# Kernel optimization log

Measured on AMD Instinct MI355X. Metric: run time of the kernel, lower is better.

## Reference

```python
import jax, jax.numpy as jnp
import numpy as np

B, N, D = 2, 8192, 1024
H, DH = 16, 64
SEG = 512          # total_segment_len (num_longterm_mem_tokens = 0)
P = 16             # num_persist_mem_tokens
EPS = 1.1920929e-07  # torch RMSNorm eps=None -> finfo(float32).eps


def _rope(x, pos, theta=10000.0):
    # rotary-embedding-torch style: interleaved pairs, freqs repeated (n r), r=2
    d = x.shape[-1]
    inv_freq = 1.0 / (theta ** (jnp.arange(0, d, 2, dtype=jnp.float32) / d))  # [d/2]
    ang = pos[:, None] * inv_freq                                             # [n, d/2]
    cos = jnp.repeat(jnp.cos(ang), 2, axis=-1)                                # [n, d]
    sin = jnp.repeat(jnp.sin(ang), 2, axis=-1)
    x1, x2 = x[..., 0::2], x[..., 1::2]
    rot = jnp.stack((-x2, x1), axis=-1).reshape(x.shape)
    return x * cos + rot * sin


def setup_inputs() -> dict:
    key = jax.random.key(0)
    ks = jax.random.split(key, 5)
    return {
        "seq": jax.random.normal(ks[0], (B, N, D), dtype=jnp.float32),
        "w_norm": 1.0 + 0.02 * jax.random.normal(ks[1], (D,), dtype=jnp.float32),
        "Wqkv": jax.random.normal(ks[2], (D, 3 * H * DH), dtype=jnp.float32) * (D ** -0.5),
        "Wout": jax.random.normal(ks[3], (H * DH, D), dtype=jnp.float32) * ((H * DH) ** -0.5),
        "pm": 0.02 * jax.random.normal(ks[4], (2, H, P, DH), dtype=jnp.float32),
    }


def reference(seq, w_norm, Wqkv, Wout, pm):
    b, n, d = seq.shape
    w = n // SEG  # n is a multiple of SEG by construction

    # RMSNorm
    x = seq * jax.lax.rsqrt(jnp.mean(seq * seq, axis=-1, keepdims=True) + EPS) * w_norm

    # QKV projection, split heads -> [b, h, n, dh]
    qkv = x @ Wqkv
    q, k, v = jnp.split(qkv, 3, axis=-1)
    split = lambda t: t.reshape(b, n, H, DH).transpose(0, 2, 1, 3)
    q, k, v = split(q), split(k), split(v)

    # RoPE on full (global) positions before segmenting
    pos = jnp.arange(n, dtype=jnp.float32)
    q = _rope(q, pos)
    k = _rope(k, pos)

    # Segment: [b, h, n, dh] -> [b*w, h, SEG, dh]
    seg = lambda t: t.reshape(b, H, w, SEG, DH).transpose(0, 2, 1, 3, 4).reshape(b * w, H, SEG, DH)
    q, k, v = seg(q), seg(k), seg(v)

    # Prepend persistent memory KVs
    pmk = jnp.broadcast_to(pm[0], (b * w, H, P, DH))
    pmv = jnp.broadcast_to(pm[1], (b * w, H, P, DH))
    k = jnp.concatenate((pmk, k), axis=-2)  # [b*w, h, P+SEG, dh]
    v = jnp.concatenate((pmv, v), axis=-2)

    # Causal attention with kv offset P (persistent tokens always visible)
    scale = DH ** -0.5
    scores = jnp.einsum('bhid,bhjd->bhij', q, k) * scale  # [b*w, h, SEG, P+SEG]
    mask = (jnp.arange(P + SEG) - P)[None, :] <= jnp.arange(SEG)[:, None]
    scores = jnp.where(mask, scores, jnp.finfo(scores.dtype).min)
    attn = jax.nn.softmax(scores, axis=-1)
    out = jnp.einsum('bhij,bhjd->bhid', attn, v)  # [b*w, h, SEG, dh]

    # Merge heads, un-segment, output projection
    out = out.transpose(0, 2, 1, 3).reshape(b * w, SEG, H * DH)
    out = out @ Wout
    out = out.reshape(b, n, -1)
    return out
```

## Files before the change

kernel.cpp:

```cpp
#include <hip/hip_runtime.h>
#include <hip/hip_bf16.h>
#include <stdint.h>
#include <stddef.h>

typedef _Float16 f16;
typedef __attribute__((ext_vector_type(8))) _Float16 f16x8;
typedef __attribute__((ext_vector_type(4))) _Float16 f16x4;
typedef __attribute__((ext_vector_type(4))) float f32x4;
typedef __attribute__((ext_vector_type(16))) float f32x16;

#define MFMA_F16(a, b, c) __builtin_amdgcn_mfma_f32_16x16x32_f16(a, b, c, 0, 0, 0)
#define MFMA32_F16(a, b, c) __builtin_amdgcn_mfma_f32_32x32x16_f16(a, b, c, 0, 0, 0)

#define LOG2_10K_32 0.41524101186092025f

__device__ __forceinline__ uint32_t swz(uint32_t ci) {
    return (ci & ~7u) | ((ci ^ (ci >> 3)) & 7u);
}

__device__ __forceinline__ void async_ld16(void* lds, const void* g) {
    __builtin_amdgcn_global_load_lds(
        (const __attribute__((address_space(1))) void*)g,
        (__attribute__((address_space(3))) void*)lds, 16, 0, 0);
}

__global__ __launch_bounds__(256) void k_transpose_cast(
        const float* __restrict__ S, f16* __restrict__ D, int rows, int cols) {
    __shared__ float tile[32][33];
    int x = threadIdx.x & 31, y = threadIdx.x >> 5;
    int c0 = blockIdx.x * 32, r0 = blockIdx.y * 32;
#pragma unroll
    for (int i = 0; i < 32; i += 8)
        tile[y + i][x] = S[(size_t)(r0 + y + i) * cols + c0 + x];
    __syncthreads();
#pragma unroll
    for (int i = 0; i < 32; i += 8)
        D[(size_t)(c0 + y + i) * rows + r0 + x] = (f16)tile[x][y + i];
}

__global__ __launch_bounds__(256) void k_rmsnorm(
        const float* __restrict__ seq, const float* __restrict__ w, f16* __restrict__ X) {
    int row = blockIdx.x, t = threadIdx.x;
    const float4* sp = (const float4*)(seq + (size_t)row * 1024);
    float4 v = sp[t];
    float ss = v.x * v.x + v.y * v.y + v.z * v.z + v.w * v.w;
#pragma unroll
    for (int off = 32; off >= 1; off >>= 1) ss += __shfl_xor(ss, off, 64);
    __shared__ float red[4];
    if ((t & 63) == 0) red[t >> 6] = ss;
    __syncthreads();
    float tot = red[0] + red[1] + red[2] + red[3];
    float rs = rsqrtf(tot * (1.0f / 1024.0f) + 1.1920929e-07f);
    const float4* wp = (const float4*)w;
    float4 wv = wp[t];
    f16x4 o;
    o[0] = (f16)(v.x * rs * wv.x);
    o[1] = (f16)(v.y * rs * wv.y);
    o[2] = (f16)(v.z * rs * wv.z);
    o[3] = (f16)(v.w * rs * wv.w);
    *(f16x4*)(X + (size_t)row * 1024 + t * 4) = o;
}

__global__ __launch_bounds__(256) void k_gemm_qkv(
        const f16* __restrict__ A, const f16* __restrict__ BT,
        f16* __restrict__ Qb, f16* __restrict__ Kb, f16* __restrict__ Vt) {
    const int K = 1024;
    __shared__ f16 As[128 * 32];
    __shared__ f16 Bs[128 * 32];
    const int t = threadIdx.x;
    const int lane = t & 63, wave = t >> 6, l32 = lane & 31, half = lane >> 5;
    const int m0 = blockIdx.y * 128, n0 = blockIdx.x * 128;
    const int wm = (wave & 1) * 64, wn = (wave >> 1) * 64;
    f32x16 acc[2][2];
#pragma unroll
    for (int i = 0; i < 2; i++)
#pragma unroll
        for (int j = 0; j < 2; j++)
#pragma unroll
            for (int r = 0; r < 16; r++) acc[i][j][r] = 0.f;

    uint32_t aoff[2][2], boff[2][2];
#pragma unroll
    for (int bk = 0; bk < 2; bk++)
#pragma unroll
        for (int ks = 0; ks < 2; ks++) {
            aoff[bk][ks] = swz((uint32_t)(wm + bk * 32 + l32) * 4 + ks * 2 + half) * 16;
            boff[bk][ks] = swz((uint32_t)(wn + bk * 32 + l32) * 4 + ks * 2 + half) * 16;
        }
    uint32_t c0 = swz(t), c1 = swz(t + 256);
    const f16* Ag0 = A + (size_t)(m0 + (c0 >> 2)) * K + (c0 & 3) * 8;
    const f16* Ag1 = A + (size_t)(m0 + (c1 >> 2)) * K + (c1 & 3) * 8;
    const f16* Bg0 = BT + (size_t)(n0 + (c0 >> 2)) * K + (c0 & 3) * 8;
    const f16* Bg1 = BT + (size_t)(n0 + (c1 >> 2)) * K + (c1 & 3) * 8;
    char* AsB = (char*)As;
    char* BsB = (char*)Bs;

    for (int k0 = 0; k0 < K; k0 += 32) {
        __syncthreads();
        async_ld16(AsB + t * 16, Ag0 + k0);
        async_ld16(AsB + (t + 256) * 16, Ag1 + k0);
        async_ld16(BsB + t * 16, Bg0 + k0);
        async_ld16(BsB + (t + 256) * 16, Bg1 + k0);
        __builtin_amdgcn_s_waitcnt(0x0f70);
        __syncthreads();
        f16x8 a[2][2], b[2][2];
#pragma unroll
        for (int bk = 0; bk < 2; bk++)
#pragma unroll
            for (int ks = 0; ks < 2; ks++) {
                a[bk][ks] = *(const f16x8*)(AsB + aoff[bk][ks]);
                b[bk][ks] = *(const f16x8*)(BsB + boff[bk][ks]);
            }
#pragma unroll
        for (int mb = 0; mb < 2; mb++)
#pragma unroll
            for (int nb = 0; nb < 2; nb++) {
                acc[mb][nb] = MFMA32_F16(b[nb][0], a[mb][0], acc[mb][nb]);
                acc[mb][nb] = MFMA32_F16(b[nb][1], a[mb][1], acc[mb][nb]);
            }
    }

    const int region = n0 >> 10;
#pragma unroll
    for (int mb = 0; mb < 2; mb++) {
        int row = m0 + wm + mb * 32 + l32;
        int b_ = row >> 13, n_ = row & 8191;
        int win = n_ >> 9, i_ = n_ & 511;
        float fn = (float)n_;
#pragma unroll
        for (int nb = 0; nb < 2; nb++) {
            int colb = n0 + wn + nb * 32 + half * 4;
            int cr = colb & 1023;
            int h = cr >> 6;
            int d0 = cr & 63;
            int wh = ((b_ * 16 + win) << 4) + h;
            if (region < 2) {
                f16* base = (region == 0)
                    ? (Qb + ((size_t)wh * 512 + i_) * 64)
                    : (Kb + ((size_t)wh * 576 + 16 + i_) * 64);
#pragma unroll
                for (int q = 0; q < 4; q++) {
                    int d = d0 + q * 8;
                    float j0f = (float)(d >> 1);
                    float ang0 = fn * exp2f(-LOG2_10K_32 * j0f);
                    float ang1 = fn * exp2f(-LOG2_10K_32 * (j0f + 1.0f));
                    float s0, c0f, s1, c1f;
                    sincosf(ang0, &s0, &c0f);
                    sincosf(ang1, &s1, &c1f);
                    float x0 = (float)(f16)acc[mb][nb][q * 4 + 0];
                    float x1 = (float)(f16)acc[mb][nb][q * 4 + 1];
                    float x2 = (float)(f16)acc[mb][nb][q * 4 + 2];
                    float x3 = (float)(f16)acc[mb][nb][q * 4 + 3];
                    f16x4 ov;
                    ov[0] = (f16)(x0 * c0f - x1 * s0);
                    ov[1] = (f16)(x1 * c0f + x0 * s0);
                    ov[2] = (f16)(x2 * c1f - x3 * s1);
                    ov[3] = (f16)(x3 * c1f + x2 * s1);
                    *(f16x4*)(base + d) = ov;
                }
            } else {
                f16* vbase = Vt + (size_t)wh * 36864 + 16 + i_;
#pragma unroll
                for (int q = 0; q < 4; q++)
#pragma unroll
                    for (int r = 0; r < 4; r++)
                        vbase[(size_t)(d0 + q * 8 + r) * 576] = (f16)acc[mb][nb][q * 4 + r];
            }
        }
    }
}

__global__ __launch_bounds__(256) void k_gemm_out(
        const f16* __restrict__ A, const f16* __restrict__ BT,
        float* __restrict__ C, int M, int N, int K) {
    __shared__ f16 As[128 * 32];
    __shared__ f16 Bs[128 * 32];
    const int t = threadIdx.x;
    const int lane = t & 63, wave = t >> 6, l32 = lane & 31, half = lane >> 5;
    const int m0 = blockIdx.y * 128, n0 = blockIdx.x * 128;
    const int wm = (wave & 1) * 64, wn = (wave >> 1) * 64;
    f32x16 acc[2][2];
#pragma unroll
    for (int i = 0; i < 2; i++)
#pragma unroll
        for (int j = 0; j < 2; j++)
#pragma unroll
            for (int r = 0; r < 16; r++) acc[i][j][r] = 0.f;

    uint32_t aoff[2][2], boff[2][2];
#pragma unroll
    for (int bk = 0; bk < 2; bk++)
#pragma unroll
        for (int ks = 0; ks < 2; ks++) {
            aoff[bk][ks] = swz((uint32_t)(wm + bk * 32 + l32) * 4 + ks * 2 + half) * 16;
            boff[bk][ks] = swz((uint32_t)(wn + bk * 32 + l32) * 4 + ks * 2 + half) * 16;
        }
    uint32_t c0 = swz(t), c1 = swz(t + 256);
    const f16* Ag0 = A + (size_t)(m0 + (c0 >> 2)) * K + (c0 & 3) * 8;
    const f16* Ag1 = A + (size_t)(m0 + (c1 >> 2)) * K + (c1 & 3) * 8;
    const f16* Bg0 = BT + (size_t)(n0 + (c0 >> 2)) * K + (c0 & 3) * 8;
    const f16* Bg1 = BT + (size_t)(n0 + (c1 >> 2)) * K + (c1 & 3) * 8;
    char* AsB = (char*)As;
    char* BsB = (char*)Bs;

    for (int k0 = 0; k0 < K; k0 += 32) {
        __syncthreads();
        async_ld16(AsB + t * 16, Ag0 + k0);
        async_ld16(AsB + (t + 256) * 16, Ag1 + k0);
        async_ld16(BsB + t * 16, Bg0 + k0);
        async_ld16(BsB + (t + 256) * 16, Bg1 + k0);
        __builtin_amdgcn_s_waitcnt(0x0f70);
        __syncthreads();
        f16x8 a[2][2], b[2][2];
#pragma unroll
        for (int bk = 0; bk < 2; bk++)
#pragma unroll
            for (int ks = 0; ks < 2; ks++) {
                a[bk][ks] = *(const f16x8*)(AsB + aoff[bk][ks]);
                b[bk][ks] = *(const f16x8*)(BsB + boff[bk][ks]);
            }
#pragma unroll
        for (int mb = 0; mb < 2; mb++)
#pragma unroll
            for (int nb = 0; nb < 2; nb++) {
                acc[mb][nb] = MFMA32_F16(b[nb][0], a[mb][0], acc[mb][nb]);
                acc[mb][nb] = MFMA32_F16(b[nb][1], a[mb][1], acc[mb][nb]);
            }
    }
#pragma unroll
    for (int mb = 0; mb < 2; mb++) {
        int row = m0 + wm + mb * 32 + l32;
#pragma unroll
        for (int nb = 0; nb < 2; nb++) {
            int colb = n0 + wn + nb * 32 + half * 4;
#pragma unroll
            for (int q = 0; q < 4; q++) {
                f32x4 ov;
#pragma unroll
                for (int r = 0; r < 4; r++) ov[r] = acc[mb][nb][q * 4 + r];
                *(f32x4*)(C + (size_t)row * N + colb + q * 8) = ov;
            }
        }
    }
}

__global__ __launch_bounds__(256) void k_pmpad(
        const float* __restrict__ pm, f16* __restrict__ Kb, f16* __restrict__ Vt) {
    int wh = blockIdx.x, h = wh & 15, t = threadIdx.x;
    const float* pk = pm + (size_t)h * 1024;
    f16* kb = Kb + (size_t)wh * 36864;
    int e0 = t * 4;
#pragma unroll
    for (int k = 0; k < 4; k++) kb[e0 + k] = (f16)pk[e0 + k];
#pragma unroll
    for (int k = 0; k < 12; k++) kb[33792 + t + k * 256] = (f16)0.f;
    const float* pv = pm + 16384 + (size_t)h * 1024;
    f16* vb = Vt + (size_t)wh * 36864;
    {
        int d = t & 63, s4 = (t >> 6) * 4;
#pragma unroll
        for (int k = 0; k < 4; k++)
            vb[(size_t)d * 576 + s4 + k] = (f16)pv[(s4 + k) * 64 + d];
    }
    {
        int d = t >> 2, rep = t & 3;
#pragma unroll
        for (int m = 0; m < 12; m++)
            vb[(size_t)d * 576 + 528 + rep * 12 + m] = (f16)0.f;
    }
}

__global__ __launch_bounds__(512) void k_attn(
        const f16* __restrict__ Q, const f16* __restrict__ Kb,
        const f16* __restrict__ Vt, f16* __restrict__ AO) {
    const int bid = blockIdx.x;
    const int wh = ((bid >> 5) << 3) | (bid & 7);
    const int pair = (bid >> 3) & 3;
    const int i0 = pair * 128;
    const int t = threadIdx.x, lane = t & 63, wave = t >> 6, quad = lane >> 4, l16 = lane & 15;
    __shared__ f16 Ks[64 * 64];
    __shared__ f16 Vs[64 * 64];
    __shared__ f16 Ps[8][16][80];

    const int ig = i0 + wave * 16 + l16;
    const f16* qptr = Q + ((size_t)wh * 512 + ig) * 64 + quad * 8;
    f16x8 qf0 = *(const f16x8*)(qptr);
    f16x8 qf1 = *(const f16x8*)(qptr + 32);

    const f32x4 zero = {0.f, 0.f, 0.f, 0.f};
    f32x4 o[4];
#pragma unroll
    for (int i = 0; i < 4; i++) o[i] = zero;
    float m_l = -1e30f, l_l = 0.f;

    uint32_t g = swz((uint32_t)t);
    const f16* kg0 = Kb + ((size_t)wh * 576 + (g >> 3)) * 64 + (g & 7) * 8;
    const f16* vg0 = Vt + ((size_t)wh * 64 + (g >> 3)) * 576 + (g & 7) * 8;
    char* KsB = (char*)Ks;
    char* VsB = (char*)Vs;

    uint32_t boff[4][2];
#pragma unroll
    for (int i = 0; i < 4; i++)
#pragma unroll
        for (int f = 0; f < 2; f++)
            boff[i][f] = swz((uint32_t)(i * 16 + l16) * 8 + f * 4 + quad) * 16;

    f16* psrow = &Ps[wave][l16][0];
    int njt = 2 * pair + 3;
    if (njt > 9) njt = 9;

    const int jcap = (ig + 16 < 527) ? (ig + 16) : 527;

    f16x8 kreg = *(const f16x8*)(kg0);
    f16x8 vreg = *(const f16x8*)(vg0);

    for (int jt = 0; jt < njt; jt++) {
        const int j0 = jt * 64;
        __builtin_amdgcn_sched_barrier(0);
        __builtin_amdgcn_s_barrier();
        __builtin_amdgcn_sched_barrier(0);
        *(f16x8*)(KsB + t * 16) = kreg;
        *(f16x8*)(VsB + t * 16) = vreg;
        if (jt + 1 < njt) {
            kreg = *(const f16x8*)(kg0 + (size_t)(j0 + 64) * 64);
            vreg = *(const f16x8*)(vg0 + (j0 + 64));
        }
        __builtin_amdgcn_s_waitcnt(0xc07f);
        __builtin_amdgcn_sched_barrier(0);
        __builtin_amdgcn_s_barrier();
        __builtin_amdgcn_sched_barrier(0);

        f32x4 s[4];
#pragma unroll
        for (int jb = 0; jb < 4; jb++) {
            f16x8 kv0 = *(const f16x8*)(KsB + boff[jb][0]);
            f16x8 kv1 = *(const f16x8*)(KsB + boff[jb][1]);
            f32x4 z = zero;
            z = MFMA_F16(kv0, qf0, z);
            z = MFMA_F16(kv1, qf1, z);
            s[jb] = z;
        }

        const bool fullt = (j0 + 63 <= i0 + wave * 16 + 16) && (j0 + 64 <= 528);
        float mx = -1e30f;
        if (fullt) {
#pragma unroll
            for (int jb = 0; jb < 4; jb++)
#pragma unroll
                for (int r = 0; r < 4; r++) {
                    float val = s[jb][r] * 0.125f;
                    s[jb][r] = val;
                    mx = fmaxf(mx, val);
                }
        } else {
#pragma unroll
            for (int jb = 0; jb < 4; jb++)
#pragma unroll
                for (int r = 0; r < 4; r++) {
                    int jg = j0 + jb * 16 + quad * 4 + r;
                    float val = (jg <= jcap) ? s[jb][r] * 0.125f : -1e30f;
                    s[jb][r] = val;
                    mx = fmaxf(mx, val);
                }
        }
        mx = fmaxf(mx, __shfl_xor(mx, 16, 64));
        mx = fmaxf(mx, __shfl_xor(mx, 32, 64));
        const bool skipresc = __all(mx <= m_l);
        float mnew = fmaxf(m_l, mx);
        float alpha = 1.0f;
        if (!skipresc) alpha = __expf(m_l - mnew);
        m_l = mnew;
        float rsum = 0.f;
#pragma unroll
        for (int jb = 0; jb < 4; jb++) {
            f16x4 pw;
#pragma unroll
            for (int r = 0; r < 4; r++) {
                float p = __expf(s[jb][r] - mnew);
                rsum += p;
                pw[r] = (f16)p;
            }
            *(f16x4*)(psrow + jb * 16 + quad * 4) = pw;
        }
        rsum += __shfl_xor(rsum, 16, 64);
        rsum += __shfl_xor(rsum, 32, 64);
        if (skipresc) {
            l_l = l_l + rsum;
        } else {
            l_l = l_l * alpha + rsum;
#pragma unroll
            for (int nd = 0; nd < 4; nd++) o[nd] *= alpha;
        }

        __builtin_amdgcn_s_waitcnt(0xc07f);
        __builtin_amdgcn_sched_barrier(0);

        f16x8 pb0 = *(const f16x8*)(psrow + quad * 8);
        f16x8 pb1 = *(const f16x8*)(psrow + 32 + quad * 8);
#pragma unroll
        for (int nd = 0; nd < 4; nd++) {
            f16x8 v0 = *(const f16x8*)(VsB + boff[nd][0]);
            f16x8 v1 = *(const f16x8*)(VsB + boff[nd][1]);
            o[nd] = MFMA_F16(v0, pb0, o[nd]);
            o[nd] = MFMA_F16(v1, pb1, o[nd]);
        }
    }

    const int bw = wh >> 4, h = wh & 15;
    float inv = 1.f / l_l;
    f16* dst = AO + ((size_t)bw * 512 + ig) * 1024 + h * 64 + quad * 4;
#pragma unroll
    for (int nd = 0; nd < 4; nd++) {
        f16x4 ov;
#pragma unroll
        for (int r = 0; r < 4; r++) ov[r] = (f16)(o[nd][r] * inv);
        *(f16x4*)(dst + nd * 16) = ov;
    }
}

extern "C" void kernel_launch(void* const* d_in, const int* in_sizes, int n_in,
                              void* d_out, int out_size, void* d_ws, size_t ws_size,
                              hipStream_t stream) {
    const float* seq   = (const float*)d_in[0];
    const float* wnorm = (const float*)d_in[1];
    const float* Wqkv  = (const float*)d_in[2];
    const float* Wout  = (const float*)d_in[3];
    const float* pm    = (const float*)d_in[4];
    float* out = (float*)d_out;
    char* ws = (char*)d_ws;

    f16* WqkvT = (f16*)(ws + 0);
    f16* WoutT = (f16*)(ws + 6291456);
    f16* X     = (f16*)(ws + 8388608);
    f16* Qb    = (f16*)(ws + 41943040);
    f16* AO    = (f16*)(ws + 75497472);
    f16* Kb    = (f16*)(ws + 109051904);
    f16* Vt    = (f16*)(ws + 146800640);

    k_transpose_cast<<<dim3(96, 32), 256, 0, stream>>>(Wqkv, WqkvT, 1024, 3072);
    k_transpose_cast<<<dim3(32, 32), 256, 0, stream>>>(Wout, WoutT, 1024, 1024);
    k_rmsnorm<<<16384, 256, 0, stream>>>(seq, wnorm, X);
    k_pmpad<<<512, 256, 0, stream>>>(pm, Kb, Vt);
    k_gemm_qkv<<<dim3(24, 128), 256, 0, stream>>>(X, WqkvT, Qb, Kb, Vt);
    k_attn<<<2048, 512, 0, stream>>>(Qb, Kb, Vt, AO);
    k_gemm_out<<<dim3(8, 128), 256, 0, stream>>>(AO, WoutT, out, 16384, 1024, 1024);
}
```

Before: 407.4 us.

## Merge prep kernels and rewrite output GEMM with 256x256 tiles and 4-stage pipeline

Fuses the two weight transpose-casts into one launch and folds the persistent-memory padding into the RMSNorm launch, which cuts launch count. The output projection GEMM moves from 128x128 tiles with a single LDS buffer to 256x256 tiles on 512 threads. It adds a 4-stage async global-to-LDS ring with prefetch distance 3, split barriers that overlap loads with MFMA, and setprio around the MFMA groups. The larger tile gives only 256 blocks and needs 128KB of LDS per block, so occupancy and the tail effect become risks.

```diff
diff --git a/kernel.cpp b/kernel.cpp
--- a/kernel.cpp
+++ b/kernel.cpp
@@ -24,11 +24,18 @@
         (__attribute__((address_space(3))) void*)lds, 16, 0, 0);
 }
 
-__global__ __launch_bounds__(256) void k_transpose_cast(
-        const float* __restrict__ S, f16* __restrict__ D, int rows, int cols) {
+__global__ __launch_bounds__(256) void k_prep_w(
+        const float* __restrict__ Wqkv, const float* __restrict__ Wout,
+        f16* __restrict__ WqkvT, f16* __restrict__ WoutT) {
     __shared__ float tile[32][33];
     int x = threadIdx.x & 31, y = threadIdx.x >> 5;
-    int c0 = blockIdx.x * 32, r0 = blockIdx.y * 32;
+    int bx = blockIdx.x;
+    const float* S;
+    f16* D;
+    int rows, cols, bxe;
+    if (bx < 96) { S = Wqkv; D = WqkvT; rows = 1024; cols = 3072; bxe = bx; }
+    else         { S = Wout; D = WoutT; rows = 1024; cols = 1024; bxe = bx - 96; }
+    int c0 = bxe * 32, r0 = blockIdx.y * 32;
 #pragma unroll
     for (int i = 0; i < 32; i += 8)
         tile[y + i][x] = S[(size_t)(r0 + y + i) * cols + c0 + x];
@@ -38,27 +45,53 @@
         D[(size_t)(c0 + y + i) * rows + r0 + x] = (f16)tile[x][y + i];
 }
 
-__global__ __launch_bounds__(256) void k_rmsnorm(
-        const float* __restrict__ seq, const float* __restrict__ w, f16* __restrict__ X) {
-    int row = blockIdx.x, t = threadIdx.x;
-    const float4* sp = (const float4*)(seq + (size_t)row * 1024);
-    float4 v = sp[t];
-    float ss = v.x * v.x + v.y * v.y + v.z * v.z + v.w * v.w;
-#pragma unroll
-    for (int off = 32; off >= 1; off >>= 1) ss += __shfl_xor(ss, off, 64);
+__global__ __launch_bounds__(256) void k_prep_x(
+        const float* __restrict__ seq, const float* __restrict__ w, f16* __restrict__ X,
+        const float* __restrict__ pm, f16* __restrict__ Kb, f16* __restrict__ Vt) {
     __shared__ float red[4];
-    if ((t & 63) == 0) red[t >> 6] = ss;
-    __syncthreads();
-    float tot = red[0] + red[1] + red[2] + red[3];
-    float rs = rsqrtf(tot * (1.0f / 1024.0f) + 1.1920929e-07f);
-    const float4* wp = (const float4*)w;
-    float4 wv = wp[t];
-    f16x4 o;
-    o[0] = (f16)(v.x * rs * wv.x);
-    o[1] = (f16)(v.y * rs * wv.y);
-    o[2] = (f16)(v.z * rs * wv.z);
-    o[3] = (f16)(v.w * rs * wv.w);
-    *(f16x4*)(X + (size_t)row * 1024 + t * 4) = o;
+    const int b = blockIdx.x, t = threadIdx.x;
+    if (b < 16384) {
+        const float4* sp = (const float4*)(seq + (size_t)b * 1024);
+        float4 v = sp[t];
+        float ss = v.x * v.x + v.y * v.y + v.z * v.z + v.w * v.w;
+#pragma unroll
+        for (int off = 32; off >= 1; off >>= 1) ss += __shfl_xor(ss, off, 64);
+        if ((t & 63) == 0) red[t >> 6] = ss;
+        __syncthreads();
+        float tot = red[0] + red[1] + red[2] + red[3];
+        float rs = rsqrtf(tot * (1.0f / 1024.0f) + 1.1920929e-07f);
+        const float4* wp = (const float4*)w;
+        float4 wv = wp[t];
+        f16x4 o;
+        o[0] = (f16)(v.x * rs * wv.x);
+        o[1] = (f16)(v.y * rs * wv.y);
+        o[2] = (f16)(v.z * rs * wv.z);
+        o[3] = (f16)(v.w * rs * wv.w);
+        *(f16x4*)(X + (size_t)b * 1024 + t * 4) = o;
+    } else {
+        int wh = b - 16384, h = wh & 15;
+        const float* pk = pm + (size_t)h * 1024;
+        f16* kb = Kb + (size_t)wh * 36864;
+        int e0 = t * 4;
+#pragma unroll
+        for (int k = 0; k < 4; k++) kb[e0 + k] = (f16)pk[e0 + k];
+#pragma unroll
+        for (int k = 0; k < 12; k++) kb[33792 + t + k * 256] = (f16)0.f;
+        const float* pv = pm + 16384 + (size_t)h * 1024;
+        f16* vb = Vt + (size_t)wh * 36864;
+        {
+            int d = t & 63, s4 = (t >> 6) * 4;
+#pragma unroll
+            for (int k = 0; k < 4; k++)
+                vb[(size_t)d * 576 + s4 + k] = (f16)pv[(s4 + k) * 64 + d];
+        }
+        {
+            int d = t >> 2, rep = t & 3;
+#pragma unroll
+            for (int m = 0; m < 12; m++)
+                vb[(size_t)d * 576 + 528 + rep * 12 + m] = (f16)0.f;
+        }
+    }
 }
 
 __global__ __launch_bounds__(256) void k_gemm_qkv(
@@ -170,65 +203,115 @@
     }
 }
 
-__global__ __launch_bounds__(256) void k_gemm_out(
+__global__ __launch_bounds__(512, 2) void k_gemm_out(
         const f16* __restrict__ A, const f16* __restrict__ BT,
-        float* __restrict__ C, int M, int N, int K) {
-    __shared__ f16 As[128 * 32];
-    __shared__ f16 Bs[128 * 32];
+        float* __restrict__ C, int M, int N, int Kp) {
+    const int K = 1024;
+    const int NT = 32;
+    __shared__ __align__(16) char ldsA[65536];
+    __shared__ __align__(16) char ldsB[65536];
     const int t = threadIdx.x;
     const int lane = t & 63, wave = t >> 6, l32 = lane & 31, half = lane >> 5;
-    const int m0 = blockIdx.y * 128, n0 = blockIdx.x * 128;
-    const int wm = (wave & 1) * 64, wn = (wave >> 1) * 64;
-    f32x16 acc[2][2];
-#pragma unroll
-    for (int i = 0; i < 2; i++)
+    const int m0 = blockIdx.y * 256, n0 = blockIdx.x * 256;
+    const int wm = (wave >> 2) * 128, wn = (wave & 3) * 64;
+
+    f32x16 acc[4][2];
+#pragma unroll
+    for (int i = 0; i < 4; i++)
 #pragma unroll
         for (int j = 0; j < 2; j++)
 #pragma unroll
             for (int r = 0; r < 16; r++) acc[i][j][r] = 0.f;
 
-    uint32_t aoff[2][2], boff[2][2];
-#pragma unroll
-    for (int bk = 0; bk < 2; bk++)
-#pragma unroll
-        for (int ks = 0; ks < 2; ks++) {
-            aoff[bk][ks] = swz((uint32_t)(wm + bk * 32 + l32) * 4 + ks * 2 + half) * 16;
-            boff[bk][ks] = swz((uint32_t)(wn + bk * 32 + l32) * 4 + ks * 2 + half) * 16;
-        }
-    uint32_t c0 = swz(t), c1 = swz(t + 256);
-    const f16* Ag0 = A + (size_t)(m0 + (c0 >> 2)) * K + (c0 & 3) * 8;
-    const f16* Ag1 = A + (size_t)(m0 + (c1 >> 2)) * K + (c1 & 3) * 8;
-    const f16* Bg0 = BT + (size_t)(n0 + (c0 >> 2)) * K + (c0 & 3) * 8;
-    const f16* Bg1 = BT + (size_t)(n0 + (c1 >> 2)) * K + (c1 & 3) * 8;
-    char* AsB = (char*)As;
-    char* BsB = (char*)Bs;
-
-    for (int k0 = 0; k0 < K; k0 += 32) {
-        __syncthreads();
-        async_ld16(AsB + t * 16, Ag0 + k0);
-        async_ld16(AsB + (t + 256) * 16, Ag1 + k0);
-        async_ld16(BsB + t * 16, Bg0 + k0);
-        async_ld16(BsB + (t + 256) * 16, Bg1 + k0);
-        __builtin_amdgcn_s_waitcnt(0x0f70);
-        __syncthreads();
-        f16x8 a[2][2], b[2][2];
-#pragma unroll
-        for (int bk = 0; bk < 2; bk++)
-#pragma unroll
-            for (int ks = 0; ks < 2; ks++) {
-                a[bk][ks] = *(const f16x8*)(AsB + aoff[bk][ks]);
-                b[bk][ks] = *(const f16x8*)(BsB + boff[bk][ks]);
-            }
-#pragma unroll
-        for (int mb = 0; mb < 2; mb++)
-#pragma unroll
-            for (int nb = 0; nb < 2; nb++) {
-                acc[mb][nb] = MFMA32_F16(b[nb][0], a[mb][0], acc[mb][nb]);
-                acc[mb][nb] = MFMA32_F16(b[nb][1], a[mb][1], acc[mb][nb]);
-            }
-    }
-#pragma unroll
-    for (int mb = 0; mb < 2; mb++) {
+    uint32_t aoff[4][2], boff[2][2];
+#pragma unroll
+    for (int mb = 0; mb < 4; mb++)
+#pragma unroll
+        for (int ks = 0; ks < 2; ks++)
+            aoff[mb][ks] = swz((uint32_t)(wm + mb * 32 + l32) * 4 + ks * 2 + half) * 16;
+#pragma unroll
+    for (int nb = 0; nb < 2; nb++)
+#pragma unroll
+        for (int ks = 0; ks < 2; ks++)
+            boff[nb][ks] = swz((uint32_t)(wn + nb * 32 + l32) * 4 + ks * 2 + half) * 16;
+
+    uint32_t g0 = swz((uint32_t)t), g1 = swz((uint32_t)t + 512);
+    const f16* Ag0 = A + (size_t)(m0 + (g0 >> 2)) * K + (g0 & 3) * 8;
+    const f16* Ag1 = A + (size_t)(m0 + (g1 >> 2)) * K + (g1 & 3) * 8;
+    const f16* Bg0 = BT + (size_t)(n0 + (g0 >> 2)) * K + (g0 & 3) * 8;
+    const f16* Bg1 = BT + (size_t)(n0 + (g1 >> 2)) * K + (g1 & 3) * 8;
+
+#pragma unroll
+    for (int p = 0; p < 3; ++p) {
+        char* dA = ldsA + p * 16384;
+        async_ld16(dA + t * 16, Ag0 + p * 32);
+        async_ld16(dA + (t + 512) * 16, Ag1 + p * 32);
+        char* dB = ldsB + p * 16384;
+        async_ld16(dB + t * 16, Bg0 + p * 32);
+        async_ld16(dB + (t + 512) * 16, Bg1 + p * 32);
+    }
+    __builtin_amdgcn_s_waitcnt(0x0f78);
+    __builtin_amdgcn_s_barrier();
+    __builtin_amdgcn_sched_barrier(0);
+
+#pragma unroll 4
+    for (int kt = 0; kt < NT; ++kt) {
+        char* As_s = ldsA + (kt & 3) * 16384;
+        char* Bs_s = ldsB + (kt & 3) * 16384;
+        f16x8 a00 = *(const f16x8*)(As_s + aoff[0][0]);
+        f16x8 a01 = *(const f16x8*)(As_s + aoff[0][1]);
+        f16x8 a10 = *(const f16x8*)(As_s + aoff[1][0]);
+        f16x8 a11 = *(const f16x8*)(As_s + aoff[1][1]);
+        f16x8 b00 = *(const f16x8*)(Bs_s + boff[0][0]);
+        f16x8 b01 = *(const f16x8*)(Bs_s + boff[0][1]);
+        f16x8 b10 = *(const f16x8*)(Bs_s + boff[1][0]);
+        f16x8 b11 = *(const f16x8*)(Bs_s + boff[1][1]);
+        if (kt < NT - 3) {
+            char* dA = ldsA + ((kt + 3) & 3) * 16384;
+            async_ld16(dA + t * 16, Ag0 + (kt + 3) * 32);
+            async_ld16(dA + (t + 512) * 16, Ag1 + (kt + 3) * 32);
+        }
+        __builtin_amdgcn_s_barrier();
+        __builtin_amdgcn_s_setprio(1);
+        acc[0][0] = MFMA32_F16(b00, a00, acc[0][0]);
+        acc[0][0] = MFMA32_F16(b01, a01, acc[0][0]);
+        acc[0][1] = MFMA32_F16(b10, a00, acc[0][1]);
+        acc[0][1] = MFMA32_F16(b11, a01, acc[0][1]);
+        acc[1][0] = MFMA32_F16(b00, a10, acc[1][0]);
+        acc[1][0] = MFMA32_F16(b01, a11, acc[1][0]);
+        acc[1][1] = MFMA32_F16(b10, a10, acc[1][1]);
+        acc[1][1] = MFMA32_F16(b11, a11, acc[1][1]);
+        __builtin_amdgcn_s_setprio(0);
+        __builtin_amdgcn_s_barrier();
+        f16x8 a20 = *(const f16x8*)(As_s + aoff[2][0]);
+        f16x8 a21 = *(const f16x8*)(As_s + aoff[2][1]);
+        f16x8 a30 = *(const f16x8*)(As_s + aoff[3][0]);
+        f16x8 a31 = *(const f16x8*)(As_s + aoff[3][1]);
+        if (kt < NT - 3) {
+            char* dB = ldsB + ((kt + 3) & 3) * 16384;
+            async_ld16(dB + t * 16, Bg0 + (kt + 3) * 32);
+            async_ld16(dB + (t + 512) * 16, Bg1 + (kt + 3) * 32);
+        }
+        __builtin_amdgcn_s_barrier();
+        __builtin_amdgcn_s_setprio(1);
+        acc[2][0] = MFMA32_F16(b00, a20, acc[2][0]);
+        acc[2][0] = MFMA32_F16(b01, a21, acc[2][0]);
+        acc[2][1] = MFMA32_F16(b10, a20, acc[2][1]);
+        acc[2][1] = MFMA32_F16(b11, a21, acc[2][1]);
+        acc[3][0] = MFMA32_F16(b00, a30, acc[3][0]);
+        acc[3][0] = MFMA32_F16(b01, a31, acc[3][0]);
+        acc[3][1] = MFMA32_F16(b10, a30, acc[3][1]);
+        acc[3][1] = MFMA32_F16(b11, a31, acc[3][1]);
+        __builtin_amdgcn_s_setprio(0);
+        if (kt < NT - 3)       __builtin_amdgcn_s_waitcnt(0x0f78);
+        else if (kt == NT - 3) __builtin_amdgcn_s_waitcnt(0x0f74);
+        else if (kt == NT - 2) __builtin_amdgcn_s_waitcnt(0x0f70);
+        __builtin_amdgcn_s_barrier();
+        __builtin_amdgcn_sched_barrier(0);
+    }
+
+#pragma unroll
+    for (int mb = 0; mb < 4; mb++) {
         int row = m0 + wm + mb * 32 + l32;
 #pragma unroll
         for (int nb = 0; nb < 2; nb++) {
@@ -242,32 +325,7 @@
             }
         }
     }
-}
-
-__global__ __launch_bounds__(256) void k_pmpad(
-        const float* __restrict__ pm, f16* __restrict__ Kb, f16* __restrict__ Vt) {
-    int wh = blockIdx.x, h = wh & 15, t = threadIdx.x;
-    const float* pk = pm + (size_t)h * 1024;
-    f16* kb = Kb + (size_t)wh * 36864;
-    int e0 = t * 4;
-#pragma unroll
-    for (int k = 0; k < 4; k++) kb[e0 + k] = (f16)pk[e0 + k];
-#pragma unroll
-    for (int k = 0; k < 12; k++) kb[33792 + t + k * 256] = (f16)0.f;
-    const float* pv = pm + 16384 + (size_t)h * 1024;
-    f16* vb = Vt + (size_t)wh * 36864;
-    {
-        int d = t & 63, s4 = (t >> 6) * 4;
-#pragma unroll
-        for (int k = 0; k < 4; k++)
-            vb[(size_t)d * 576 + s4 + k] = (f16)pv[(s4 + k) * 64 + d];
-    }
-    {
-        int d = t >> 2, rep = t & 3;
-#pragma unroll
-        for (int m = 0; m < 12; m++)
-            vb[(size_t)d * 576 + 528 + rep * 12 + m] = (f16)0.f;
-    }
+    (void)M; (void)Kp;
 }
 
 __global__ __launch_bounds__(512) void k_attn(
@@ -438,11 +496,9 @@
     f16* Kb    = (f16*)(ws + 109051904);
     f16* Vt    = (f16*)(ws + 146800640);
 
-    k_transpose_cast<<<dim3(96, 32), 256, 0, stream>>>(Wqkv, WqkvT, 1024, 3072);
-    k_transpose_cast<<<dim3(32, 32), 256, 0, stream>>>(Wout, WoutT, 1024, 1024);
-    k_rmsnorm<<<16384, 256, 0, stream>>>(seq, wnorm, X);
-    k_pmpad<<<512, 256, 0, stream>>>(pm, Kb, Vt);
+    k_prep_w<<<dim3(128, 32), 256, 0, stream>>>(Wqkv, Wout, WqkvT, WoutT);
+    k_prep_x<<<16896, 256, 0, stream>>>(seq, wnorm, X, pm, Kb, Vt);
     k_gemm_qkv<<<dim3(24, 128), 256, 0, stream>>>(X, WqkvT, Qb, Kb, Vt);
     k_attn<<<2048, 512, 0, stream>>>(Qb, Kb, Vt, AO);
-    k_gemm_out<<<dim3(8, 128), 256, 0, stream>>>(AO, WoutT, out, 16384, 1024, 1024);
-}
+    k_gemm_out<<<dim3(4, 64), 512, 0, stream>>>(AO, WoutT, out, 16384, 1024, 1024);
+}
```

After: 407.0 us. About the same (-0.1%).
